# Optimization experiments

Measured on AMD Instinct MI355X. Metric: run time of the kernel, lower is better.

## Reference

```python
import jax, jax.numpy as jnp
import numpy as np

C = 512
NUM_GROUPS = 32
EPS = 1e-6


def setup_inputs() -> dict:
    key = jax.random.key(0)
    ks = jax.random.split(key, 10)
    x = jax.random.normal(ks[0], (2, C, 64, 64), dtype=jnp.float32)
    s = 1.0 / np.sqrt(C)
    return {
        "x": x,
        "gn_gamma": jnp.ones((C,), jnp.float32),
        "gn_beta": jnp.zeros((C,), jnp.float32),
        "wq": jax.random.normal(ks[1], (C, C), jnp.float32) * s,
        "bq": jnp.zeros((C,), jnp.float32),
        "wk": jax.random.normal(ks[2], (C, C), jnp.float32) * s,
        "bk": jnp.zeros((C,), jnp.float32),
        "wv": jax.random.normal(ks[3], (C, C), jnp.float32) * s,
        "bv": jnp.zeros((C,), jnp.float32),
        "wo": jax.random.normal(ks[4], (C, C), jnp.float32) * s,
        "bo": jnp.zeros((C,), jnp.float32),
    }


def group_norm(x, gamma, beta):
    b, c, h, w = x.shape
    xg = x.reshape(b, NUM_GROUPS, c // NUM_GROUPS, h, w)
    mean = xg.mean(axis=(2, 3, 4), keepdims=True)
    var = xg.var(axis=(2, 3, 4), keepdims=True)
    xg = (xg - mean) * jax.lax.rsqrt(var + EPS)
    x = xg.reshape(b, c, h, w)
    return x * gamma[None, :, None, None] + beta[None, :, None, None]


def conv1x1(x, w, bias):
    # 1x1 conv == channel matmul: (b,c,h,w),(o,c) -> (b,o,h,w)
    return jnp.einsum('bchw,oc->bohw', x, w) + bias[None, :, None, None]


def reference(x, gn_gamma, gn_beta, wq, bq, wk, bk, wv, bv, wo, bo):
    b, c, h, w = x.shape
    hn = group_norm(x, gn_gamma, gn_beta)
    q = conv1x1(hn, wq, bq).reshape(b, c, h * w)  # (b,c,n)
    k = conv1x1(hn, wk, bk).reshape(b, c, h * w)
    v = conv1x1(hn, wv, bv).reshape(b, c, h * w)
    scale = int(c) ** (-0.5)
    # scores[b,i,j] = sum_c q[b,c,i] k[b,c,j]
    scores = jnp.einsum('bci,bcj->bij', q, k) * scale
    attn = jax.nn.softmax(scores, axis=2)
    out = jnp.einsum('bcj,bij->bci', v, attn).reshape(b, c, h, w)
    out = conv1x1(out, wo, bo)
    return x + out
```

## Files before the change

kernel.cpp:

```cpp
#include <hip/hip_runtime.h>

typedef unsigned short ushort_t;
typedef unsigned char uchar_t;
typedef __bf16 bf16x8 __attribute__((ext_vector_type(8)));
typedef float f32x4 __attribute__((ext_vector_type(4)));

__device__ __forceinline__ ushort_t f2bf(float f) {
  unsigned u = __float_as_uint(f);
  u += 0x7fff + ((u >> 16) & 1);
  return (ushort_t)(u >> 16);
}

__device__ __forceinline__ void gload16(const void* g, void* l) {
  __builtin_amdgcn_global_load_lds(
      (const __attribute__((address_space(1))) unsigned int*)g,
      (__attribute__((address_space(3))) unsigned int*)l, 16, 0, 0);
}

__global__ __launch_bounds__(256) void cvt_weights(
    const float* __restrict__ wq, const float* __restrict__ wk,
    const float* __restrict__ wv, const float* __restrict__ wo,
    const float* __restrict__ bq, const float* __restrict__ bk,
    ushort_t* __restrict__ dst, float* __restrict__ qkbias,
    float* __restrict__ stats2) {
  int b = blockIdx.x, t = threadIdx.x;
  if (b < 1024) {
    int i = b * 256 + t;
    dst[i]          = f2bf(wq[i]);
    dst[262144 + i] = f2bf(wk[i]);
    dst[524288 + i] = f2bf(wv[i]);
    dst[786432 + i] = f2bf(wo[i]);
  } else if (b < 1028) {
    int j = (b - 1024) * 256 + t;
    qkbias[j] = (j < 512) ? bq[j] : bk[j - 512];
  } else {
    if (t < 128) stats2[t] = 0.f;
  }
}

__global__ __launch_bounds__(256) void zero_f32(float* __restrict__ p) {
  p[blockIdx.x * 256 + threadIdx.x] = 0.f;
}

__global__ __launch_bounds__(256) void gn_stats_partial(const float* __restrict__ x,
                                                        float* __restrict__ stats2) {
  int bg = blockIdx.x >> 2, q = blockIdx.x & 3;
  const float4* p = (const float4*)(x + (size_t)bg * 65536 + q * 16384);
  float s = 0.f, ss = 0.f;
  for (int i = threadIdx.x; i < 4096; i += 256) {
    float4 v = p[i];
    s += v.x + v.y + v.z + v.w;
    ss += v.x * v.x + v.y * v.y + v.z * v.z + v.w * v.w;
  }
  for (int off = 32; off; off >>= 1) {
    s += __shfl_xor(s, off, 64);
    ss += __shfl_xor(ss, off, 64);
  }
  __shared__ float sh[8];
  int wave = threadIdx.x >> 6, lane = threadIdx.x & 63;
  if (lane == 0) { sh[wave] = s; sh[4 + wave] = ss; }
  __syncthreads();
  if (threadIdx.x == 0) {
    atomicAdd(&stats2[bg * 2], sh[0] + sh[1] + sh[2] + sh[3]);
    atomicAdd(&stats2[bg * 2 + 1], sh[4] + sh[5] + sh[6] + sh[7]);
  }
}

__global__ __launch_bounds__(64) void gn_finalize(const float* __restrict__ stats2,
                                                  float* __restrict__ stats) {
  int t = threadIdx.x;
  float s = stats2[t * 2], ss = stats2[t * 2 + 1];
  float mean = s * (1.f / 65536.f);
  float var = ss * (1.f / 65536.f) - mean * mean;
  stats[t * 2] = mean;
  stats[t * 2 + 1] = rsqrtf(var + 1e-6f);
}

__global__ __launch_bounds__(256) void gn_apply(
    const float* __restrict__ x, const float* __restrict__ gamma,
    const float* __restrict__ beta, const float* __restrict__ stats,
    ushort_t* __restrict__ hnT) {
  __shared__ float T[32][33];
  int i0 = blockIdx.x * 32, c0 = blockIdx.y * 32, b = blockIdx.z;
  int tx = threadIdx.x, ty = threadIdx.y;
#pragma unroll
  for (int k = 0; k < 4; k++) {
    int cl = ty + k * 8;
    int c = c0 + cl;
    int bg = (b * 32 + (c >> 4)) * 2;
    float mean = stats[bg], rstd = stats[bg + 1];
    float v = x[((size_t)(b * 512 + c)) * 4096 + i0 + tx];
    T[cl][tx] = (v - mean) * rstd * gamma[c] + beta[c];
  }
  __syncthreads();
#pragma unroll
  for (int k = 0; k < 4; k++) {
    int il = ty + k * 8;
    hnT[((size_t)b * 4096 + i0 + il) * 512 + c0 + tx] = f2bf(T[tx][il]);
  }
}

template <int BN>
__global__ __launch_bounds__(256) void gemm_abt(
    const ushort_t* __restrict__ A, long long sA, int lda,
    const ushort_t* __restrict__ B, long long sB, int ldb,
    int K, int N, int ldc,
    ushort_t* __restrict__ outB, long long sC,
    const float* __restrict__ bias, int bias_mode, float scale,
    float* __restrict__ outF, const float* __restrict__ resid,
    float* __restrict__ rowsum, const float* __restrict__ colscale,
    int swiz, int omode) {
  constexpr int CPW = (8 + BN / 16) / 4;
  constexpr int SB = (128 + BN) * 32;
  constexpr int MI = (BN == 128) ? 4 : 2;
  constexpr int NI = 4;
  __shared__ __align__(16) ushort_t Ls[2][SB];

  int bx = blockIdx.x, by = blockIdx.y, bz = blockIdx.z;
  if (swiz) {
    unsigned nx = gridDim.x, ny = gridDim.y;
    unsigned id = (blockIdx.z * ny + blockIdx.y) * nx + blockIdx.x;
    unsigned pb8 = (nx * ny) >> 3;
    unsigned c = id & 7, j = id >> 3;
    bz = j / pb8;
    unsigned jb = j - bz * pb8;
    unsigned jy = jb / nx;
    by = c * (ny >> 3) + jy;
    bx = jb - jy * nx;
  }

  int m0 = by * 128, n0 = bx * BN;
  int t = threadIdx.x;
  int lane = t & 63;
  int quad = lane >> 4, l16 = lane & 15;
  int wave = t >> 6;
  int wm = (BN == 128) ? (wave >> 1) * 64 : wave * 32;
  int wn = (BN == 128) ? (wave & 1) * 64 : 0;

  f32x4 acc[MI][NI];
#pragma unroll
  for (int i = 0; i < MI; i++)
#pragma unroll
    for (int j = 0; j < NI; j++)
#pragma unroll
      for (int r = 0; r < 4; r++) acc[i][j][r] = 0.f;

  const ushort_t* gp[CPW];
  int lofs[CPW];
  int crow = lane >> 2, skoff = (lane & 3) * 8;
#pragma unroll
  for (int i = 0; i < CPW; i++) {
    int c = wave * CPW + i;
    if (c < 8) {
      gp[i] = A + (size_t)bz * sA + (size_t)(m0 + c * 16 + crow) * lda + skoff;
      lofs[i] = c * 1024 + lane * 16;
    } else {
      int slot = (c - 8) * 16 + crow;
      int arow = (slot & ~63) + ((slot & 15) * 4) + ((slot & 63) >> 4);
      gp[i] = B + (size_t)bz * sB + (size_t)(n0 + arow) * ldb + skoff;
      lofs[i] = 8192 + (c - 8) * 1024 + lane * 16;
    }
  }
  char* lbase = (char*)&Ls[0][0];

#pragma unroll
  for (int i = 0; i < CPW; i++) gload16(gp[i], lbase + lofs[i]);

  for (int k0 = 0; k0 < K; k0 += 32) {
    int p = (k0 >> 5) & 1;
    __syncthreads();
    if (k0 + 32 < K) {
      int pofs = (p ^ 1) * (SB * 2);
#pragma unroll
      for (int i = 0; i < CPW; i++) gload16(gp[i] + k0 + 32, lbase + pofs + lofs[i]);
    }
    bf16x8 af[MI], bfr[NI];
#pragma unroll
    for (int i = 0; i < MI; i++)
      af[i] = *(const bf16x8*)&Ls[p][(wm + i * 16 + l16) * 32 + quad * 8];
#pragma unroll
    for (int j = 0; j < NI; j++)
      bfr[j] = *(const bf16x8*)&Ls[p][4096 + (wn + j * 16 + l16) * 32 + quad * 8];
#pragma unroll
    for (int mi = 0; mi < MI; mi++)
#pragma unroll
      for (int ni = 0; ni < NI; ni++)
        acc[mi][ni] = __builtin_amdgcn_mfma_f32_16x16x32_bf16(af[mi], bfr[ni], acc[mi][ni], 0, 0, 0);
  }

  size_t cbase = (size_t)bz * sC;
  int gnb = n0 + wn + l16 * 4;
  float cs4[4] = {1.f, 1.f, 1.f, 1.f};
  if (colscale) {
    float4 c4 = *(const float4*)&colscale[(size_t)bz * N + gnb];
    cs4[0] = 1.f / c4.x; cs4[1] = 1.f / c4.y; cs4[2] = 1.f / c4.z; cs4[3] = 1.f / c4.w;
  }
  float b4[4] = {0.f, 0.f, 0.f, 0.f};
  if (bias_mode == 2) {
    float4 t4 = *(const float4*)&bias[gnb];
    b4[0] = t4.x; b4[1] = t4.y; b4[2] = t4.z; b4[3] = t4.w;
  }
#pragma unroll
  for (int mi = 0; mi < MI; mi++) {
#pragma unroll
    for (int r = 0; r < 4; r++) {
      int m = m0 + wm + mi * 16 + quad * 4 + r;
      float rbias = (bias_mode == 1) ? bias[m] : 0.f;
      float v4[4];
      float rs = 0.f;
#pragma unroll
      for (int ni = 0; ni < NI; ni++) {
        float val = acc[mi][ni][r];
        if (colscale) val *= cs4[ni];
        val += (bias_mode == 2) ? b4[ni] : rbias;
        val *= scale;
        if (rowsum) { val = __expf(val) * 0.0625f; rs += val; }
        v4[ni] = val;
      }
      size_t idx = cbase + (size_t)m * ldc + gnb;
      if (omode == 1) {
        float4 rv = *(const float4*)&resid[idx];
        float4 ov = make_float4(v4[0] + rv.x, v4[1] + rv.y, v4[2] + rv.z, v4[3] + rv.w);
        *(float4*)&outF[idx] = ov;
      } else if (omode == 2) {
        unsigned w = __builtin_amdgcn_cvt_pk_fp8_f32(v4[0], v4[1], 0u, false);
        w = __builtin_amdgcn_cvt_pk_fp8_f32(v4[2], v4[3], w, true);
        *(unsigned*)&((uchar_t*)outB)[idx] = w;
      } else {
        unsigned lo = (unsigned)f2bf(v4[0]) | ((unsigned)f2bf(v4[1]) << 16);
        unsigned hi = (unsigned)f2bf(v4[2]) | ((unsigned)f2bf(v4[3]) << 16);
        *(uint2*)&outB[idx] = make_uint2(lo, hi);
      }
      if (rowsum) {
        rs += __shfl_xor(rs, 1, 64);
        rs += __shfl_xor(rs, 2, 64);
        rs += __shfl_xor(rs, 4, 64);
        rs += __shfl_xor(rs, 8, 64);
        if (l16 == 0) atomicAdd(&rowsum[(size_t)bz * 4096 + m], rs);
      }
    }
  }
}

template <int BN>
__global__ __launch_bounds__(256) void gemm_fp8(
    const uchar_t* __restrict__ A, long long sA, int lda,
    const uchar_t* __restrict__ B, long long sB, int ldb,
    int K, int ldc,
    void* __restrict__ outp, long long sC,
    float scale, float* __restrict__ rowsum, int swiz, int omode) {
  constexpr int CPW = (8 + BN / 16) / 4;
  constexpr int SBB = (128 + BN) * 64;
  constexpr int MI = (BN == 128) ? 4 : 2;
  constexpr int NI = 4;
  __shared__ __align__(16) uchar_t Ls[2][SBB];

  int bx = blockIdx.x, by = blockIdx.y, bz = blockIdx.z;
  if (swiz) {
    unsigned nx = gridDim.x, ny = gridDim.y;
    unsigned id = (blockIdx.z * ny + blockIdx.y) * nx + blockIdx.x;
    unsigned pb8 = (nx * ny) >> 3;
    unsigned c = id & 7, j = id >> 3;
    bz = j / pb8;
    unsigned jb = j - bz * pb8;
    unsigned jy = jb / nx;
    by = c * (ny >> 3) + jy;
    bx = jb - jy * nx;
  }

  int m0 = by * 128, n0 = bx * BN;
  int t = threadIdx.x;
  int lane = t & 63;
  int quad = lane >> 4, l16 = lane & 15;
  int wave = t >> 6;
  int wm = (BN == 128) ? (wave >> 1) * 64 : wave * 32;
  int wn = (BN == 128) ? (wave & 1) * 64 : 0;

  f32x4 acc[MI][NI];
#pragma unroll
  for (int i = 0; i < MI; i++)
#pragma unroll
    for (int j = 0; j < NI; j++)
#pragma unroll
      for (int r = 0; r < 4; r++) acc[i][j][r] = 0.f;

  const uchar_t* gp[CPW];
  int lofs[CPW];
  int r16 = lane & 15, sseg = (lane >> 4) * 16;
#pragma unroll
  for (int i = 0; i < CPW; i++) {
    int c = wave * CPW + i;
    if (c < 8) {
      gp[i] = A + (size_t)bz * sA + (size_t)(m0 + c * 16 + r16) * lda + sseg;
      lofs[i] = c * 1024 + lane * 16;
    } else {
      int slot = (c - 8) * 16 + r16;
      int arow = (slot & ~63) + ((slot & 15) * 4) + ((slot & 63) >> 4);
      gp[i] = B + (size_t)bz * sB + (size_t)(n0 + arow) * ldb + sseg;
      lofs[i] = 8192 + (c - 8) * 1024 + lane * 16;
    }
  }
  char* lbase = (char*)&Ls[0][0];

#pragma unroll
  for (int i = 0; i < CPW; i++) gload16(gp[i], lbase + lofs[i]);

  int vbase = l16 * 16 + (quad >> 1) * 256 + (quad & 1) * 8;
  for (int k0 = 0; k0 < K; k0 += 64) {
    int p = (k0 >> 6) & 1;
    __syncthreads();
    if (k0 + 64 < K) {
      int pofs = (p ^ 1) * SBB;
#pragma unroll
      for (int i = 0; i < CPW; i++) gload16(gp[i] + k0 + 64, lbase + pofs + lofs[i]);
    }
    const uchar_t* Lp = &Ls[p][0];
    long long af[2][MI], bfv[2][NI];
#pragma unroll
    for (int s = 0; s < 2; s++) {
#pragma unroll
      for (int i = 0; i < MI; i++)
        af[s][i] = *(const long long*)&Lp[wm * 64 + i * 1024 + s * 512 + vbase];
#pragma unroll
      for (int j = 0; j < NI; j++)
        bfv[s][j] = *(const long long*)&Lp[8192 + wn * 64 + j * 1024 + s * 512 + vbase];
    }
#pragma unroll
    for (int s = 0; s < 2; s++)
#pragma unroll
      for (int mi = 0; mi < MI; mi++)
#pragma unroll
        for (int ni = 0; ni < NI; ni++)
          acc[mi][ni] = __builtin_amdgcn_mfma_f32_16x16x32_fp8_fp8(af[s][mi], bfv[s][ni], acc[mi][ni], 0, 0, 0);
  }

  size_t cbase = (size_t)bz * sC;
  int gnb = n0 + wn + l16 * 4;
#pragma unroll
  for (int mi = 0; mi < MI; mi++) {
#pragma unroll
    for (int r = 0; r < 4; r++) {
      int m = m0 + wm + mi * 16 + quad * 4 + r;
      if (omode == 2) {
        float v4[4];
        float rs = 0.f;
#pragma unroll
        for (int ni = 0; ni < NI; ni++) {
          v4[ni] = __expf(acc[mi][ni][r] * scale) * 0.0625f;
          rs += v4[ni];
        }
        unsigned w = __builtin_amdgcn_cvt_pk_fp8_f32(v4[0], v4[1], 0u, false);
        w = __builtin_amdgcn_cvt_pk_fp8_f32(v4[2], v4[3], w, true);
        *(unsigned*)&((uchar_t*)outp)[cbase + (size_t)m * ldc + gnb] = w;
        rs += __shfl_xor(rs, 1, 64);
        rs += __shfl_xor(rs, 2, 64);
        rs += __shfl_xor(rs, 4, 64);
        rs += __shfl_xor(rs, 8, 64);
        if (l16 == 0) atomicAdd(&rowsum[(size_t)bz * 4096 + m], rs);
      } else {
        unsigned lo = (unsigned)f2bf(acc[mi][0][r]) | ((unsigned)f2bf(acc[mi][1][r]) << 16);
        unsigned hi = (unsigned)f2bf(acc[mi][2][r]) | ((unsigned)f2bf(acc[mi][3][r]) << 16);
        *(uint2*)&((ushort_t*)outp)[cbase + (size_t)m * ldc + gnb] = make_uint2(lo, hi);
      }
    }
  }
}

extern "C" void kernel_launch(void* const* d_in, const int* in_sizes, int n_in,
                              void* d_out, int out_size, void* d_ws, size_t ws_size,
                              hipStream_t stream) {
  const float* x     = (const float*)d_in[0];
  const float* gamma = (const float*)d_in[1];
  const float* beta  = (const float*)d_in[2];
  const float* wq    = (const float*)d_in[3];
  const float* bq    = (const float*)d_in[4];
  const float* wk    = (const float*)d_in[5];
  const float* bk    = (const float*)d_in[6];
  const float* wv    = (const float*)d_in[7];
  const float* bv    = (const float*)d_in[8];
  const float* wo    = (const float*)d_in[9];
  const float* bo    = (const float*)d_in[10];
  float* out = (float*)d_out;

  ushort_t* wb  = (ushort_t*)d_ws;
  ushort_t* wvb = wb + 524288;
  ushort_t* wob = wb + 786432;
  ushort_t* hnT = wb + 1048576;
  uchar_t*  qk8 = (uchar_t*)(hnT + 4194304);
  uchar_t*  vC8 = qk8 + 8388608;
  ushort_t* OT  = (ushort_t*)(vC8 + 4194304);
  uchar_t*  S8  = (uchar_t*)(OT + 4194304);
  float* fbuf   = (float*)(S8 + 33554432);
  float* stats  = fbuf;
  float* stats2 = fbuf + 128;
  float* qkbias = fbuf + 256;
  float* l      = (float*)hnT;

  const long long HS = 2097152;
  const long long QS = 4194304;
  const long long SS = 16777216;
  const float scale = 0.044194173824159216f;

  cvt_weights<<<dim3(1029), dim3(256), 0, stream>>>(wq, wk, wv, wo, bq, bk, wb, qkbias, stats2);
  gn_stats_partial<<<dim3(256), dim3(256), 0, stream>>>(x, stats2);
  gn_finalize<<<dim3(1), dim3(64), 0, stream>>>(stats2, stats);
  gn_apply<<<dim3(128, 16, 2), dim3(32, 8), 0, stream>>>(x, gamma, beta, stats, hnT);
  gemm_abt<128><<<dim3(8, 32, 2), dim3(256), 0, stream>>>(
      hnT, HS, 512, wb, 0, 512, 512, 1024, 1024, (ushort_t*)qk8, QS, qkbias, 2, 1.f,
      nullptr, nullptr, nullptr, nullptr, 1, 2);
  gemm_abt<64><<<dim3(64, 4, 2), dim3(256), 0, stream>>>(
      wvb, 0, 512, hnT, HS, 512, 512, 4096, 4096, (ushort_t*)vC8, HS, bv, 1, 1.f,
      nullptr, nullptr, nullptr, nullptr, 0, 2);
  zero_f32<<<dim3(32), dim3(256), 0, stream>>>(l);
  gemm_fp8<128><<<dim3(32, 32, 2), dim3(256), 0, stream>>>(
      qk8, QS, 1024, qk8 + 512, QS, 1024, 512, 4096, S8, SS, scale, l, 1, 2);
  gemm_fp8<64><<<dim3(8, 32, 2), dim3(256), 0, stream>>>(
      S8, SS, 4096, vC8, HS, 4096, 4096, 512, OT, HS, 1.f, nullptr, 1, 0);
  gemm_abt<64><<<dim3(64, 4, 2), dim3(256), 0, stream>>>(
      wob, 0, 512, OT, HS, 512, 512, 4096, 4096, nullptr, HS, bo, 1, 1.f,
      out, x, nullptr, l, 0, 1);
}
```

Before: 239.4 us.

## Halve fp8 GEMM K-step to 32 and raise occupancy via smaller LDS tiles

Each iteration of the fp8 GEMM main loop now covers a K-step of 32 instead of 64, which halves the LDS stage size and the per-thread fragment registers. The launch bound is raised to request 8 blocks per CU. The global-to-LDS load mapping is rewritten as a flat per-thread 16-byte layout with a guard for partial tiles, keeping the B-row permutation. The aim is more resident blocks to hide memory latency, at the cost of twice as many loop iterations and barriers and less MFMA work between each sync.

```diff
diff --git a/kernel.cpp b/kernel.cpp
--- a/kernel.cpp
+++ b/kernel.cpp
@@ -243,14 +243,16 @@
 }
 
 template <int BN>
-__global__ __launch_bounds__(256) void gemm_fp8(
+__global__ __launch_bounds__(256, 8) void gemm_fp8(
     const uchar_t* __restrict__ A, long long sA, int lda,
     const uchar_t* __restrict__ B, long long sB, int ldb,
     int K, int ldc,
     void* __restrict__ outp, long long sC,
     float scale, float* __restrict__ rowsum, int swiz, int omode) {
-  constexpr int CPW = (8 + BN / 16) / 4;
-  constexpr int SBB = (128 + BN) * 64;
+  constexpr int ROWS = 128 + BN;
+  constexpr int SBB = ROWS * 32;
+  constexpr int NP = (SBB + 4095) / 4096;
+  constexpr bool EXACT = (SBB % 4096) == 0;
   constexpr int MI = (BN == 128) ? 4 : 2;
   constexpr int NI = 4;
   __shared__ __align__(16) uchar_t Ls[2][SBB];
@@ -284,54 +286,54 @@
 #pragma unroll
       for (int r = 0; r < 4; r++) acc[i][j][r] = 0.f;
 
-  const uchar_t* gp[CPW];
-  int lofs[CPW];
-  int r16 = lane & 15, sseg = (lane >> 4) * 16;
-#pragma unroll
-  for (int i = 0; i < CPW; i++) {
-    int c = wave * CPW + i;
-    if (c < 8) {
-      gp[i] = A + (size_t)bz * sA + (size_t)(m0 + c * 16 + r16) * lda + sseg;
-      lofs[i] = c * 1024 + lane * 16;
+  const uchar_t* gp[NP];
+  int lofs[NP];
+  bool act[NP];
+#pragma unroll
+  for (int i = 0; i < NP; i++) {
+    int o = i * 4096 + t * 16;
+    act[i] = EXACT || (o < SBB);
+    int oo = act[i] ? o : 0;
+    int row = oo >> 5, seg = oo & 16;
+    if (row < 128) {
+      gp[i] = A + (size_t)bz * sA + (size_t)(m0 + row) * lda + seg;
     } else {
-      int slot = (c - 8) * 16 + r16;
-      int arow = (slot & ~63) + ((slot & 15) * 4) + ((slot & 63) >> 4);
-      gp[i] = B + (size_t)bz * sB + (size_t)(n0 + arow) * ldb + sseg;
-      lofs[i] = 8192 + (c - 8) * 1024 + lane * 16;
-    }
+      int br = row - 128;
+      int g = br & ~63, loc = br & 63;
+      int ar = g + (loc & 15) * 4 + (loc >> 4);
+      gp[i] = B + (size_t)bz * sB + (size_t)(n0 + ar) * ldb + seg;
+    }
+    lofs[i] = oo;
   }
   char* lbase = (char*)&Ls[0][0];
 
 #pragma unroll
-  for (int i = 0; i < CPW; i++) gload16(gp[i], lbase + lofs[i]);
-
-  int vbase = l16 * 16 + (quad >> 1) * 256 + (quad & 1) * 8;
-  for (int k0 = 0; k0 < K; k0 += 64) {
-    int p = (k0 >> 6) & 1;
+  for (int i = 0; i < NP; i++)
+    if (act[i]) gload16(gp[i], lbase + lofs[i]);
+
+  int vb = l16 * 32 + quad * 8;
+  for (int k0 = 0; k0 < K; k0 += 32) {
+    int p = (k0 >> 5) & 1;
     __syncthreads();
-    if (k0 + 64 < K) {
+    if (k0 + 32 < K) {
       int pofs = (p ^ 1) * SBB;
 #pragma unroll
-      for (int i = 0; i < CPW; i++) gload16(gp[i] + k0 + 64, lbase + pofs + lofs[i]);
+      for (int i = 0; i < NP; i++)
+        if (act[i]) gload16(gp[i] + k0 + 32, lbase + pofs + lofs[i]);
     }
     const uchar_t* Lp = &Ls[p][0];
-    long long af[2][MI], bfv[2][NI];
-#pragma unroll
-    for (int s = 0; s < 2; s++) {
-#pragma unroll
-      for (int i = 0; i < MI; i++)
-        af[s][i] = *(const long long*)&Lp[wm * 64 + i * 1024 + s * 512 + vbase];
-#pragma unroll
-      for (int j = 0; j < NI; j++)
-        bfv[s][j] = *(const long long*)&Lp[8192 + wn * 64 + j * 1024 + s * 512 + vbase];
-    }
-#pragma unroll
-    for (int s = 0; s < 2; s++)
-#pragma unroll
-      for (int mi = 0; mi < MI; mi++)
-#pragma unroll
-        for (int ni = 0; ni < NI; ni++)
-          acc[mi][ni] = __builtin_amdgcn_mfma_f32_16x16x32_fp8_fp8(af[s][mi], bfv[s][ni], acc[mi][ni], 0, 0, 0);
+    long long af[MI], bfv[NI];
+#pragma unroll
+    for (int i = 0; i < MI; i++)
+      af[i] = *(const long long*)&Lp[wm * 32 + i * 512 + vb];
+#pragma unroll
+    for (int j = 0; j < NI; j++)
+      bfv[j] = *(const long long*)&Lp[4096 + wn * 32 + j * 512 + vb];
+#pragma unroll
+    for (int mi = 0; mi < MI; mi++)
+#pragma unroll
+      for (int ni = 0; ni < NI; ni++)
+        acc[mi][ni] = __builtin_amdgcn_mfma_f32_16x16x32_fp8_fp8(af[mi], bfv[ni], acc[mi][ni], 0, 0, 0);
   }
 
   size_t cbase = (size_t)bz * sC;
```

Measured after the change: 487.7 us. 2.04x slower.
